# Performance work log

Measured on AMD Instinct MI355X. Metric: run time of the kernel, lower is better.

The kernel has to match this reference:

```python
import jax, jax.numpy as jnp
import numpy as np

D_MODEL = 4096
N_Q_HEAD = 32
N_KV_HEAD = 8
HEAD_DIM = D_MODEL // N_Q_HEAD  # 128
N_REP = N_Q_HEAD // N_KV_HEAD   # 4
B, T = 2, 2048


def _rope_tables(seq_len, head_dim, dtype=jnp.float32):
    # theta_i = 10000^(-2*(i-1)/d) for i=1..d/2  (matches torch.pow(10000, -2*(arange(1,d/2+1)-1)/d))
    i = jnp.arange(head_dim // 2, dtype=dtype)
    theta = jnp.power(10000.0, -2.0 * i / head_dim)
    angles = jnp.outer(jnp.arange(seq_len, dtype=dtype), theta)  # [T, d/2]
    return jnp.cos(angles), jnp.sin(angles)


def _apply_rope(x, cos, sin):
    # x: [B, T, h, HD]; pairs are consecutive elements (view_as_complex semantics)
    B_, T_, h, hd = x.shape
    xp = x.reshape(B_, T_, h, hd // 2, 2)
    xr, xi = xp[..., 0], xp[..., 1]
    c = cos[None, :T_, None, :]
    s = sin[None, :T_, None, :]
    out_r = xr * c - xi * s
    out_i = xr * s + xi * c
    return jnp.stack([out_r, out_i], axis=-1).reshape(B_, T_, h, hd)


def setup_inputs() -> dict:
    key = jax.random.key(0)
    ks = jax.random.split(key, 5)
    scale = 0.02
    x = jax.random.normal(ks[0], (B, T, D_MODEL), dtype=jnp.float32)
    wq = jax.random.normal(ks[1], (D_MODEL, N_Q_HEAD * HEAD_DIM), dtype=jnp.float32) * scale
    wk = jax.random.normal(ks[2], (D_MODEL, N_KV_HEAD * HEAD_DIM), dtype=jnp.float32) * scale
    wv = jax.random.normal(ks[3], (D_MODEL, N_KV_HEAD * HEAD_DIM), dtype=jnp.float32) * scale
    wo = jax.random.normal(ks[4], (N_Q_HEAD * HEAD_DIM, D_MODEL), dtype=jnp.float32) * scale
    # causal mask: 1 where masked (strict upper triangle), per masked_fill(mask==1, -inf)
    attention_mask = jnp.triu(jnp.ones((T, T), dtype=jnp.int32), k=1)
    return {"x": x, "wq": wq, "wk": wk, "wv": wv, "wo": wo, "attention_mask": attention_mask}


def reference(x, wq, wk, wv, wo, attention_mask):
    B_, T_, _ = x.shape
    xq = (x @ wq).reshape(B_, T_, N_Q_HEAD, HEAD_DIM)
    xk = (x @ wk).reshape(B_, T_, N_KV_HEAD, HEAD_DIM)
    xv = (x @ wv).reshape(B_, T_, N_KV_HEAD, HEAD_DIM)

    cos, sin = _rope_tables(T_, HEAD_DIM, x.dtype)
    xq = _apply_rope(xq, cos, sin)
    xk = _apply_rope(xk, cos, sin)

    # GQA: repeat kv heads (training path: no cache)
    xk = jnp.repeat(xk, N_REP, axis=2)  # [B, T, HQ, HD]
    xv = jnp.repeat(xv, N_REP, axis=2)

    q = xq.transpose(0, 2, 1, 3)  # [B, H, T, HD]
    k = xk.transpose(0, 2, 1, 3)
    v = xv.transpose(0, 2, 1, 3)

    scores = jnp.einsum('bhqd,bhkd->bhqk', q, k) / jnp.sqrt(jnp.asarray(HEAD_DIM, x.dtype))
    scores = jnp.where(attention_mask[None, None, :, :] == 1, -jnp.inf, scores)
    probs = jax.nn.softmax(scores, axis=-1)
    out = jnp.einsum('bhqk,bhkd->bhqd', probs, v)
    out = out.transpose(0, 2, 1, 3).reshape(B_, T_, N_Q_HEAD * HEAD_DIM)
    return out @ wo
```

## Files before the change

kernel.cpp:

```cpp
#include <hip/hip_runtime.h>
#include <hip/hip_bf16.h>
#include <math.h>

typedef __hip_bfloat16 bf16;
typedef short bf16x8 __attribute__((ext_vector_type(8)));
typedef float f32x4 __attribute__((ext_vector_type(4)));
typedef unsigned int u32;
typedef unsigned short u16;

#define GLD16(g, l)                                                            \
  __builtin_amdgcn_global_load_lds(                                            \
      (const __attribute__((address_space(1))) void*)(g),                      \
      (__attribute__((address_space(3))) void*)(l), 16, 0, 0)

#define BARRIER() asm volatile("s_barrier" ::: "memory")
#define VMCNT(n) asm volatile("s_waitcnt vmcnt(" #n ")" ::: "memory")

__global__ void convert_f32_bf16(const float* __restrict__ in,
                                 bf16* __restrict__ out) {
  size_t i = ((size_t)blockIdx.x * 256 + threadIdx.x) * 4;
  float4 v = *(const float4*)(in + i);
  out[i + 0] = __float2bfloat16(v.x);
  out[i + 1] = __float2bfloat16(v.y);
  out[i + 2] = __float2bfloat16(v.z);
  out[i + 3] = __float2bfloat16(v.w);
}

__global__ void transpose_f32_bf16(const float* __restrict__ in,
                                   bf16* __restrict__ out, int R, int C) {
  __shared__ bf16 tile[32][33];
  int tx = threadIdx.x & 31, ty = threadIdx.x >> 5;
  int c0 = blockIdx.x * 32, r0 = blockIdx.y * 32;
#pragma unroll
  for (int i = 0; i < 32; i += 8)
    tile[ty + i][tx] = __float2bfloat16(in[(size_t)(r0 + ty + i) * C + c0 + tx]);
  __syncthreads();
#pragma unroll
  for (int i = 0; i < 32; i += 8)
    out[(size_t)(c0 + ty + i) * R + r0 + tx] = tile[tx][ty + i];
}

__global__ void transpose_v(const bf16* __restrict__ V, bf16* __restrict__ VT) {
  __shared__ bf16 tile[32][33];
  int s = blockIdx.z, b = s >> 3, kvh = s & 7;
  int t0 = blockIdx.x * 32, d0 = blockIdx.y * 32;
  int tx = threadIdx.x & 31, ty = threadIdx.x >> 5;
#pragma unroll
  for (int i = 0; i < 32; i += 8)
    tile[ty + i][tx] =
        V[(size_t)(b * 2048 + t0 + ty + i) * 6144 + kvh * 128 + d0 + tx];
  __syncthreads();
#pragma unroll
  for (int i = 0; i < 32; i += 8)
    VT[((size_t)s * 128 + d0 + ty + i) * 2048 + t0 + tx] = tile[tx][ty + i];
}

__global__ void rope_table_k(float* __restrict__ tab) {
  int idx = blockIdx.x * 256 + threadIdx.x;
  int t = idx >> 6, i = idx & 63;
  float theta = powf(10000.0f, -2.0f * (float)i / 128.0f);
  float ang = (float)t * theta;
  tab[idx * 2 + 0] = cosf(ang);
  tab[idx * 2 + 1] = sinf(ang);
}

__global__ void rope_apply(bf16* __restrict__ X, const float* __restrict__ tab,
                           int nheads, int rowstride, float omul) {
  size_t idx = (size_t)blockIdx.x * 256 + threadIdx.x;
  int i = (int)(idx & 63);
  size_t rest = idx >> 6;
  int h = (int)(rest % nheads);
  size_t r = rest / nheads;
  int t = (int)(r & 2047);
  float c = tab[(t * 64 + i) * 2 + 0];
  float s = tab[(t * 64 + i) * 2 + 1];
  bf16* p = X + r * (size_t)rowstride + h * 128 + 2 * i;
  float xr = __bfloat162float(p[0]), xi = __bfloat162float(p[1]);
  p[0] = __float2bfloat16((xr * c - xi * s) * omul);
  p[1] = __float2bfloat16((xr * s + xi * c) * omul);
}

template <typename OutT>
__global__ __launch_bounds__(512, 2) void gemm_bt8(const bf16* __restrict__ A,
                                                   const bf16* __restrict__ BT,
                                                   OutT* __restrict__ C, int M,
                                                   int N, int K) {
  __shared__ bf16 AS[2][2][128 * 64];
  __shared__ bf16 BS[2][2][128 * 64];

  const int tid = threadIdx.x;
  const int lane = tid & 63;
  const int w = tid >> 6, wm = w >> 2, wn = w & 3;
  const int lr = lane & 15, hi = lane >> 4;

  int gx = gridDim.x;
  int nwg = gx * gridDim.y;
  int bid = blockIdx.y * gx + blockIdx.x;
  int swz = (bid & 7) * (nwg >> 3) + (bid >> 3);
  const int m0 = (swz / gx) * 256, n0 = (swz % gx) * 256;

  const int NKT = K >> 6;
  const int NI = K >> 7;
  const int srow = tid >> 3;
  const int scol = ((tid & 7) ^ (srow & 7)) << 3;

  f32x4 acc[8][4];
#pragma unroll
  for (int m = 0; m < 8; ++m)
#pragma unroll
    for (int n = 0; n < 4; ++n)
#pragma unroll
      for (int j = 0; j < 4; ++j) acc[m][n][j] = 0.f;

  auto STAGE_A = [&](int buf, int kt) {
    int kk0 = (kt < NKT) ? kt * 64 : 0;
#pragma unroll
    for (int hs = 0; hs < 4; ++hs) {
      int ha = hs >> 1, sa = hs & 1;
      const bf16* g = A + (size_t)(m0 + ha * 128 + sa * 64 + srow) * K + kk0 + scol;
      GLD16(g, &AS[buf][ha][(sa * 64 + srow) * 64 + (tid & 7) * 8]);
    }
  };
  auto STAGE_B = [&](int buf, int kt, int half) {
    int kk0 = (kt < NKT) ? kt * 64 : 0;
#pragma unroll
    for (int sa = 0; sa < 2; ++sa) {
      const bf16* g =
          BT + (size_t)(n0 + half * 128 + sa * 64 + srow) * K + kk0 + scol;
      GLD16(g, &BS[buf][half][(sa * 64 + srow) * 64 + (tid & 7) * 8]);
    }
  };

  bf16x8 bfr[4][2], af[2][2];
  auto READ_B = [&](int buf) {
#pragma unroll
    for (int n = 0; n < 4; ++n) {
      int row = (wn & 1) * 64 + n * 16 + lr;
#pragma unroll
      for (int kk = 0; kk < 2; ++kk)
        bfr[n][kk] = *(const bf16x8*)(&BS[buf][wn >> 1]
                                         [row * 64 + (((kk * 4 + hi) ^ (row & 7)) << 3)]);
    }
  };
  auto READ_A = [&](int buf, int q) {
#pragma unroll
    for (int mm = 0; mm < 2; ++mm) {
      int row = (q * 2 + mm) * 16 + lr;
#pragma unroll
      for (int kk = 0; kk < 2; ++kk)
        af[mm][kk] = *(const bf16x8*)(&AS[buf][wm]
                                         [row * 64 + (((kk * 4 + hi) ^ (row & 7)) << 3)]);
    }
  };

#define MFMA16(q)                                                              \
  do {                                                                         \
    __builtin_amdgcn_s_setprio(1);                                             \
    _Pragma("unroll") for (int mm = 0; mm < 2; ++mm)                           \
        _Pragma("unroll") for (int n = 0; n < 4; ++n)                          \
        _Pragma("unroll") for (int kk = 0; kk < 2; ++kk)                       \
            acc[(q) * 2 + mm][n] = __builtin_amdgcn_mfma_f32_16x16x32_bf16(    \
                af[mm][kk], bfr[n][kk], acc[(q) * 2 + mm][n], 0, 0, 0);        \
    __builtin_amdgcn_s_setprio(0);                                             \
  } while (0)

  STAGE_A(0, 0);
  STAGE_B(0, 0, 0);
  STAGE_B(0, 0, 1);
  STAGE_B(1, 1, 0);
  STAGE_B(1, 1, 1);
  VMCNT(4);
  BARRIER();

  for (int i = 0; i < NI; ++i) {
    int t = 2 * i;
    READ_B(0); READ_A(0, 0); STAGE_A(1, t + 1);
    BARRIER(); MFMA16(0); BARRIER();
    READ_A(0, 1); STAGE_B(0, t + 2, 0);
    BARRIER(); MFMA16(1); BARRIER();
    READ_A(0, 2); STAGE_B(0, t + 2, 1);
    BARRIER(); MFMA16(2); BARRIER();
    READ_A(0, 3);
    BARRIER(); MFMA16(3); VMCNT(4); BARRIER();
    READ_B(1); READ_A(1, 0); STAGE_A(0, t + 2);
    BARRIER(); MFMA16(0); BARRIER();
    READ_A(1, 1); STAGE_B(1, t + 3, 0);
    BARRIER(); MFMA16(1); BARRIER();
    READ_A(1, 2); STAGE_B(1, t + 3, 1);
    BARRIER(); MFMA16(2); BARRIER();
    READ_A(1, 3);
    BARRIER(); MFMA16(3); VMCNT(4); BARRIER();
  }

  VMCNT(0);
  BARRIER();

#pragma unroll
  for (int m = 0; m < 8; ++m) {
    int row_base = m0 + wm * 128 + m * 16 + hi * 4;
#pragma unroll
    for (int n = 0; n < 4; ++n) {
      int col = n0 + wn * 64 + n * 16 + lr;
#pragma unroll
      for (int j = 0; j < 4; ++j) {
        float v = acc[m][n][j];
        if constexpr (sizeof(OutT) == 2)
          C[(size_t)(row_base + j) * N + col] = (OutT)__float2bfloat16(v);
        else
          C[(size_t)(row_base + j) * N + col] = (OutT)v;
      }
    }
  }
#undef MFMA16
}

static __device__ inline u32 cvtpk_bf16(float a, float b) {
  u32 r;
  asm("v_cvt_pk_bf16_f32 %0, %1, %2" : "=v"(r) : "v"(a), "v"(b));
  return r;
}

__global__ __launch_bounds__(256) void flash_attn2(const bf16* __restrict__ Q,
                                                   const bf16* __restrict__ K,
                                                   const bf16* __restrict__ VT,
                                                   bf16* __restrict__ AO) {
  __shared__ bf16 Kbuf[2][64 * 128];
  __shared__ bf16 Vbuf[2][128 * 64];

  int bid = blockIdx.x;
  int lid = (bid & 7) * 128 + (bid >> 3);
  int qt = 15 - (lid & 15);
  int hq = (lid >> 4) & 3;
  int kvh = (lid >> 6) & 7;
  int b = lid >> 9;
  int h = kvh * 4 + hq;

  const int tid = threadIdx.x;
  const int lane = tid & 63, w = tid >> 6;
  const int lr = lane & 15, hi = lane >> 4;
  const int ko = hi * 8;
  const int qrow0 = qt * 128 + w * 32;
  const int nt = 2 * qt + 2;

  const bf16* Kg0 = K + (size_t)b * 2048 * 6144 + kvh * 128;
  const bf16* Vg0 = VT + (size_t)(b * 8 + kvh) * 128 * 2048;

  bf16x8 qf[2][4];
#pragma unroll
  for (int mi = 0; mi < 2; ++mi) {
    const bf16* qb = Q + (size_t)(b * 2048 + qrow0 + mi * 16 + lr) * 6144 + h * 128;
#pragma unroll
    for (int kk = 0; kk < 4; ++kk) qf[mi][kk] = *(const bf16x8*)(qb + kk * 32 + ko);
  }

  f32x4 O[2][8];
  float m_[2], l_[2];
#pragma unroll
  for (int mi = 0; mi < 2; ++mi) {
    m_[mi] = -1e30f;
    l_[mi] = 0.f;
#pragma unroll
    for (int dd = 0; dd < 8; ++dd)
#pragma unroll
      for (int j = 0; j < 4; ++j) O[mi][dd][j] = 0.f;
  }

  auto STAGE = [&](int buf, int kv0) {
    bf16* Ks = &Kbuf[buf][0];
    bf16* Vs = &Vbuf[buf][0];
    const bf16* Kg = Kg0 + (size_t)kv0 * 6144;
    const bf16* Vg = Vg0 + kv0;
#pragma unroll
    for (int it = 0; it < 4; ++it) {
      int s = it * 256 + tid;
      int row = s >> 4, c = s & 15;
      GLD16(Kg + (size_t)row * 6144 + ((c ^ (row & 7)) << 3), Ks + s * 8);
    }
#pragma unroll
    for (int it = 0; it < 4; ++it) {
      int s = it * 256 + tid;
      int row = s >> 3, c = s & 7;
      GLD16(Vg + (size_t)row * 2048 + ((c ^ (row & 7)) << 3), Vs + s * 8);
    }
  };

  STAGE(0, 0);
  __syncthreads();

  for (int t = 0; t < nt; ++t) {
    int kv0 = t * 64;
    if (t + 1 < nt) STAGE((t + 1) & 1, kv0 + 64);

    if (kv0 <= qrow0 + 31) {
      const bf16* Ks = &Kbuf[t & 1][0];
      const bf16* Vs = &Vbuf[t & 1][0];

      f32x4 Sx[2][4];
#pragma unroll
      for (int mi = 0; mi < 2; ++mi)
#pragma unroll
        for (int cb = 0; cb < 4; ++cb)
#pragma unroll
          for (int j = 0; j < 4; ++j) Sx[mi][cb][j] = 0.f;

      __builtin_amdgcn_s_setprio(1);
#pragma unroll
      for (int cb = 0; cb < 4; ++cb) {
        bf16x8 kf[4];
#pragma unroll
        for (int kk = 0; kk < 4; ++kk)
          kf[kk] = *(const bf16x8*)(Ks + (cb * 16 + lr) * 128 +
                                    (((kk * 4 + hi) ^ (lr & 7)) << 3));
#pragma unroll
        for (int mi = 0; mi < 2; ++mi)
#pragma unroll
          for (int kk = 0; kk < 4; ++kk)
            Sx[mi][cb] = __builtin_amdgcn_mfma_f32_16x16x32_bf16(
                kf[kk], qf[mi][kk], Sx[mi][cb], 0, 0, 0);
      }
      __builtin_amdgcn_s_setprio(0);

      bool domask = (kv0 + 63 > qrow0);
      u32 pau[2][2][4];
#pragma unroll
      for (int mi = 0; mi < 2; ++mi) {
        int q = qrow0 + mi * 16 + lr;
        if (domask) {
#pragma unroll
          for (int cb = 0; cb < 4; ++cb)
#pragma unroll
            for (int j = 0; j < 4; ++j)
              if (kv0 + cb * 16 + hi * 4 + j > q) Sx[mi][cb][j] = -1e30f;
        }
        float pm = -1e30f;
#pragma unroll
        for (int cb = 0; cb < 4; ++cb)
#pragma unroll
          for (int j = 0; j < 4; ++j) pm = fmaxf(pm, Sx[mi][cb][j]);
        pm = fmaxf(pm, __shfl_xor(pm, 16));
        pm = fmaxf(pm, __shfl_xor(pm, 32));

        if (!__all(pm - m_[mi] <= 11.5416f)) {
          float nm = fmaxf(m_[mi], pm);
          float rs = exp2f(m_[mi] - nm);
          m_[mi] = nm;
          l_[mi] *= rs;
#pragma unroll
          for (int dd = 0; dd < 8; ++dd)
#pragma unroll
            for (int j = 0; j < 4; ++j) O[mi][dd][j] *= rs;
        }
        float mcur = m_[mi];
        float ps = 0.f;
#pragma unroll
        for (int cb = 0; cb < 4; ++cb)
#pragma unroll
          for (int j = 0; j < 4; ++j) {
            float p = exp2f(Sx[mi][cb][j] - mcur);
            Sx[mi][cb][j] = p;
            ps += p;
          }
        ps += __shfl_xor(ps, 16);
        ps += __shfl_xor(ps, 32);
        l_[mi] += ps;

        u32 vp[8];
#pragma unroll
        for (int cb = 0; cb < 4; ++cb)
#pragma unroll
          for (int jp = 0; jp < 2; ++jp)
            vp[cb * 2 + jp] = cvtpk_bf16(Sx[mi][cb][2 * jp], Sx[mi][cb][2 * jp + 1]);

#pragma unroll
        for (int kk2 = 0; kk2 < 2; ++kk2)
#pragma unroll
          for (int e = 0; e < 4; ++e) {
            int src = lr + ((hi & 1) << 5) + ((e >> 1) << 4);
            u32 va = (u32)__shfl((int)vp[4 * kk2 + (e & 1)], src);
            u32 vb = (u32)__shfl((int)vp[4 * kk2 + 2 + (e & 1)], src);
            pau[mi][kk2][e] = (hi & 2) ? vb : va;
          }
      }

      __builtin_amdgcn_s_setprio(1);
#pragma unroll
      for (int dd = 0; dd < 8; ++dd) {
        bf16x8 vf[2];
#pragma unroll
        for (int kk2 = 0; kk2 < 2; ++kk2)
          vf[kk2] = *(const bf16x8*)(Vs + (dd * 16 + lr) * 64 +
                                     (((kk2 * 4 + hi) ^ (lr & 7)) << 3));
#pragma unroll
        for (int mi = 0; mi < 2; ++mi)
#pragma unroll
          for (int kk2 = 0; kk2 < 2; ++kk2) {
            union { u32 u[4]; bf16x8 h; } cv;
#pragma unroll
            for (int e = 0; e < 4; ++e) cv.u[e] = pau[mi][kk2][e];
            O[mi][dd] = __builtin_amdgcn_mfma_f32_16x16x32_bf16(
                vf[kk2], cv.h, O[mi][dd], 0, 0, 0);
          }
      }
      __builtin_amdgcn_s_setprio(0);
    }
    __syncthreads();
  }

#pragma unroll
  for (int mi = 0; mi < 2; ++mi) {
    float inv = 1.0f / l_[mi];
    bf16* outp = AO + (size_t)(b * 2048 + qrow0 + mi * 16 + lr) * 4096 + h * 128;
#pragma unroll
    for (int dd = 0; dd < 8; ++dd) {
      union { u16 s[4]; unsigned long long v; } pk;
#pragma unroll
      for (int j = 0; j < 4; ++j)
        pk.s[j] = __bfloat16_as_ushort(__float2bfloat16(O[mi][dd][j] * inv));
      *(unsigned long long*)(outp + dd * 16 + hi * 4) = pk.v;
    }
  }
}

extern "C" void kernel_launch(void* const* d_in, const int* in_sizes, int n_in,
                              void* d_out, int out_size, void* d_ws,
                              size_t ws_size, hipStream_t stream) {
  const float* x = (const float*)d_in[0];
  const float* wq = (const float*)d_in[1];
  const float* wk = (const float*)d_in[2];
  const float* wv = (const float*)d_in[3];
  const float* wo = (const float*)d_in[4];

  char* ws = (char*)d_ws;
  bf16* xb    = (bf16*)(ws + 0);
  bf16* WqkvT = (bf16*)(ws + 33554432);
  bf16* WoT   = (bf16*)(ws + 83886080);
  bf16* QKV   = (bf16*)(ws + 117440512);
  bf16* VTb   = (bf16*)(ws + 167772160);
  float* tab  = (float*)(ws + 176160768);
  bf16* AOb   = xb;

  const float LOG2E = 1.4426950408889634f;
  const float ISQ = 0.08838834764831845f;

  convert_f32_bf16<<<16384, 256, 0, stream>>>(x, xb);
  transpose_f32_bf16<<<dim3(128, 128), 256, 0, stream>>>(wq, WqkvT, 4096, 4096);
  transpose_f32_bf16<<<dim3(32, 128), 256, 0, stream>>>(
      wk, WqkvT + (size_t)4096 * 4096, 4096, 1024);
  transpose_f32_bf16<<<dim3(32, 128), 256, 0, stream>>>(
      wv, WqkvT + (size_t)5120 * 4096, 4096, 1024);
  transpose_f32_bf16<<<dim3(128, 128), 256, 0, stream>>>(wo, WoT, 4096, 4096);
  rope_table_k<<<512, 256, 0, stream>>>(tab);

  gemm_bt8<bf16><<<dim3(24, 16), 512, 0, stream>>>(xb, WqkvT, QKV, 4096, 6144,
                                                   4096);

  rope_apply<<<32768, 256, 0, stream>>>(QKV, tab, 32, 6144, LOG2E * ISQ);
  rope_apply<<<8192, 256, 0, stream>>>(QKV + 4096, tab, 8, 6144, 1.0f);

  transpose_v<<<dim3(64, 4, 16), 256, 0, stream>>>(QKV + 5120, VTb);

  flash_attn2<<<1024, 256, 0, stream>>>(QKV, QKV + 4096, VTb, AOb);

  gemm_bt8<float><<<dim3(16, 16), 512, 0, stream>>>(AOb, WoT, (float*)d_out,
                                                    4096, 4096, 4096);
}
```

Measured before the change: 667.1 us.

## Rewrite flash attention with 32x32x16 MFMA, 256-row query tiles and 512 threads

Replaces the 16x16x32 MFMA attention kernel with one built on 32x32x16 MFMA. Each wave now owns 32 query rows as a single tile, and a block of 8 waves covers 256 query rows with 512 threads, launched as 512 blocks instead of 1024. The aim is to load each staged K/V tile once for twice as many queries and to cut cross-lane shuffles and per-row softmax bookkeeping. In exchange the grid has half as many blocks, causal load balance is coarser, and per-thread register pressure rises.

```diff
diff --git a/kernel.cpp b/kernel.cpp
--- a/kernel.cpp
+++ b/kernel.cpp
@@ -5,6 +5,7 @@
 typedef __hip_bfloat16 bf16;
 typedef short bf16x8 __attribute__((ext_vector_type(8)));
 typedef float f32x4 __attribute__((ext_vector_type(4)));
+typedef float f32x16 __attribute__((ext_vector_type(16)));
 typedef unsigned int u32;
 typedef unsigned short u16;
 
@@ -220,7 +221,7 @@
   return r;
 }
 
-__global__ __launch_bounds__(256) void flash_attn2(const bf16* __restrict__ Q,
+__global__ __launch_bounds__(512) void flash_attn3(const bf16* __restrict__ Q,
                                                    const bf16* __restrict__ K,
                                                    const bf16* __restrict__ VT,
                                                    bf16* __restrict__ AO) {
@@ -228,42 +229,36 @@
   __shared__ bf16 Vbuf[2][128 * 64];
 
   int bid = blockIdx.x;
-  int lid = (bid & 7) * 128 + (bid >> 3);
-  int qt = 15 - (lid & 15);
-  int hq = (lid >> 4) & 3;
-  int kvh = (lid >> 6) & 7;
-  int b = lid >> 9;
+  int b = bid >> 8;
+  int i = (bid >> 3) & 31;
+  int kvh = bid & 7;
+  int hq = i >> 3;
+  int qt = 7 - (i & 7);
   int h = kvh * 4 + hq;
 
   const int tid = threadIdx.x;
   const int lane = tid & 63, w = tid >> 6;
-  const int lr = lane & 15, hi = lane >> 4;
-  const int ko = hi * 8;
-  const int qrow0 = qt * 128 + w * 32;
-  const int nt = 2 * qt + 2;
+  const int ql = lane & 31, hi = lane >> 5;
+  const int qrow0 = qt * 256 + w * 32;
+  const int nt = 4 * qt + 4;
 
   const bf16* Kg0 = K + (size_t)b * 2048 * 6144 + kvh * 128;
   const bf16* Vg0 = VT + (size_t)(b * 8 + kvh) * 128 * 2048;
 
-  bf16x8 qf[2][4];
-#pragma unroll
-  for (int mi = 0; mi < 2; ++mi) {
-    const bf16* qb = Q + (size_t)(b * 2048 + qrow0 + mi * 16 + lr) * 6144 + h * 128;
-#pragma unroll
-    for (int kk = 0; kk < 4; ++kk) qf[mi][kk] = *(const bf16x8*)(qb + kk * 32 + ko);
+  bf16x8 qf[8];
+  {
+    const bf16* qb =
+        Q + (size_t)(b * 2048 + qrow0 + ql) * 6144 + h * 128 + hi * 8;
+#pragma unroll
+    for (int dc = 0; dc < 8; ++dc) qf[dc] = *(const bf16x8*)(qb + dc * 16);
   }
 
-  f32x4 O[2][8];
-  float m_[2], l_[2];
-#pragma unroll
-  for (int mi = 0; mi < 2; ++mi) {
-    m_[mi] = -1e30f;
-    l_[mi] = 0.f;
-#pragma unroll
-    for (int dd = 0; dd < 8; ++dd)
-#pragma unroll
-      for (int j = 0; j < 4; ++j) O[mi][dd][j] = 0.f;
-  }
+  f32x16 O[4];
+#pragma unroll
+  for (int d4 = 0; d4 < 4; ++d4)
+#pragma unroll
+    for (int e = 0; e < 16; ++e) O[d4][e] = 0.f;
+  float m_ = -1e30f, l_ = 0.f;
 
   auto STAGE = [&](int buf, int kv0) {
     bf16* Ks = &Kbuf[buf][0];
@@ -271,14 +266,14 @@
     const bf16* Kg = Kg0 + (size_t)kv0 * 6144;
     const bf16* Vg = Vg0 + kv0;
 #pragma unroll
-    for (int it = 0; it < 4; ++it) {
-      int s = it * 256 + tid;
+    for (int it = 0; it < 2; ++it) {
+      int s = it * 512 + tid;
       int row = s >> 4, c = s & 15;
       GLD16(Kg + (size_t)row * 6144 + ((c ^ (row & 7)) << 3), Ks + s * 8);
     }
 #pragma unroll
-    for (int it = 0; it < 4; ++it) {
-      int s = it * 256 + tid;
+    for (int it = 0; it < 2; ++it) {
+      int s = it * 512 + tid;
       int row = s >> 3, c = s & 7;
       GLD16(Vg + (size_t)row * 2048 + ((c ^ (row & 7)) << 3), Vs + s * 8);
     }
@@ -295,130 +290,115 @@
       const bf16* Ks = &Kbuf[t & 1][0];
       const bf16* Vs = &Vbuf[t & 1][0];
 
-      f32x4 Sx[2][4];
-#pragma unroll
-      for (int mi = 0; mi < 2; ++mi)
-#pragma unroll
-        for (int cb = 0; cb < 4; ++cb)
-#pragma unroll
-          for (int j = 0; j < 4; ++j) Sx[mi][cb][j] = 0.f;
+      f32x16 Sx[2];
+#pragma unroll
+      for (int cb = 0; cb < 2; ++cb)
+#pragma unroll
+        for (int e = 0; e < 16; ++e) Sx[cb][e] = 0.f;
 
       __builtin_amdgcn_s_setprio(1);
 #pragma unroll
-      for (int cb = 0; cb < 4; ++cb) {
-        bf16x8 kf[4];
-#pragma unroll
-        for (int kk = 0; kk < 4; ++kk)
-          kf[kk] = *(const bf16x8*)(Ks + (cb * 16 + lr) * 128 +
-                                    (((kk * 4 + hi) ^ (lr & 7)) << 3));
-#pragma unroll
-        for (int mi = 0; mi < 2; ++mi)
-#pragma unroll
-          for (int kk = 0; kk < 4; ++kk)
-            Sx[mi][cb] = __builtin_amdgcn_mfma_f32_16x16x32_bf16(
-                kf[kk], qf[mi][kk], Sx[mi][cb], 0, 0, 0);
+      for (int cb = 0; cb < 2; ++cb) {
+        int krow = cb * 32 + ql;
+#pragma unroll
+        for (int dc = 0; dc < 8; ++dc) {
+          bf16x8 kf = *(const bf16x8*)(Ks + krow * 128 +
+                                       (((dc * 2 + hi) ^ (ql & 7)) << 3));
+          Sx[cb] = __builtin_amdgcn_mfma_f32_32x32x16_bf16(kf, qf[dc], Sx[cb],
+                                                           0, 0, 0);
+        }
       }
       __builtin_amdgcn_s_setprio(0);
 
+      int q = qrow0 + ql;
       bool domask = (kv0 + 63 > qrow0);
-      u32 pau[2][2][4];
-#pragma unroll
-      for (int mi = 0; mi < 2; ++mi) {
-        int q = qrow0 + mi * 16 + lr;
-        if (domask) {
-#pragma unroll
-          for (int cb = 0; cb < 4; ++cb)
-#pragma unroll
-            for (int j = 0; j < 4; ++j)
-              if (kv0 + cb * 16 + hi * 4 + j > q) Sx[mi][cb][j] = -1e30f;
+      if (domask) {
+#pragma unroll
+        for (int cb = 0; cb < 2; ++cb)
+#pragma unroll
+          for (int r = 0; r < 16; ++r) {
+            int kv = kv0 + cb * 32 + (r & 3) + 8 * (r >> 2) + 4 * hi;
+            if (kv > q) Sx[cb][r] = -1e30f;
+          }
+      }
+      float pm = -1e30f;
+#pragma unroll
+      for (int cb = 0; cb < 2; ++cb)
+#pragma unroll
+        for (int r = 0; r < 16; ++r) pm = fmaxf(pm, Sx[cb][r]);
+      pm = fmaxf(pm, __shfl_xor(pm, 32));
+
+      if (!__all(pm - m_ <= 11.5416f)) {
+        float nm = fmaxf(m_, pm);
+        float rs = exp2f(m_ - nm);
+        m_ = nm;
+        l_ *= rs;
+#pragma unroll
+        for (int d4 = 0; d4 < 4; ++d4)
+#pragma unroll
+          for (int e = 0; e < 16; ++e) O[d4][e] *= rs;
+      }
+      float ps = 0.f;
+#pragma unroll
+      for (int cb = 0; cb < 2; ++cb)
+#pragma unroll
+        for (int r = 0; r < 16; ++r) {
+          float p = exp2f(Sx[cb][r] - m_);
+          Sx[cb][r] = p;
+          ps += p;
         }
-        float pm = -1e30f;
-#pragma unroll
-        for (int cb = 0; cb < 4; ++cb)
-#pragma unroll
-          for (int j = 0; j < 4; ++j) pm = fmaxf(pm, Sx[mi][cb][j]);
-        pm = fmaxf(pm, __shfl_xor(pm, 16));
-        pm = fmaxf(pm, __shfl_xor(pm, 32));
-
-        if (!__all(pm - m_[mi] <= 11.5416f)) {
-          float nm = fmaxf(m_[mi], pm);
-          float rs = exp2f(m_[mi] - nm);
-          m_[mi] = nm;
-          l_[mi] *= rs;
-#pragma unroll
-          for (int dd = 0; dd < 8; ++dd)
-#pragma unroll
-            for (int j = 0; j < 4; ++j) O[mi][dd][j] *= rs;
+      ps += __shfl_xor(ps, 32);
+      l_ += ps;
+
+      bf16x8 pb[4];
+#pragma unroll
+      for (int kb = 0; kb < 4; ++kb) {
+        int cb = kb >> 1, r0 = 8 * (kb & 1);
+        u32 Av = cvtpk_bf16(Sx[cb][r0 + 0], Sx[cb][r0 + 1]);
+        u32 Bv = cvtpk_bf16(Sx[cb][r0 + 2], Sx[cb][r0 + 3]);
+        u32 Cv = cvtpk_bf16(Sx[cb][r0 + 4], Sx[cb][r0 + 5]);
+        u32 Dv = cvtpk_bf16(Sx[cb][r0 + 6], Sx[cb][r0 + 7]);
+        u32 sA = (u32)__shfl_xor((int)Av, 32);
+        u32 sB = (u32)__shfl_xor((int)Bv, 32);
+        u32 sC = (u32)__shfl_xor((int)Cv, 32);
+        u32 sD = (u32)__shfl_xor((int)Dv, 32);
+        union { u32 u[4]; bf16x8 v; } pk;
+        pk.u[0] = hi ? sC : Av;
+        pk.u[1] = hi ? sD : Bv;
+        pk.u[2] = hi ? Cv : sA;
+        pk.u[3] = hi ? Dv : sB;
+        pb[kb] = pk.v;
+      }
+
+      __builtin_amdgcn_s_setprio(1);
+#pragma unroll
+      for (int d4 = 0; d4 < 4; ++d4) {
+        int vrow = d4 * 32 + ql;
+#pragma unroll
+        for (int kb = 0; kb < 4; ++kb) {
+          bf16x8 vf = *(const bf16x8*)(Vs + vrow * 64 +
+                                       (((kb * 2 + hi) ^ (ql & 7)) << 3));
+          O[d4] = __builtin_amdgcn_mfma_f32_32x32x16_bf16(vf, pb[kb], O[d4], 0,
+                                                          0, 0);
         }
-        float mcur = m_[mi];
-        float ps = 0.f;
-#pragma unroll
-        for (int cb = 0; cb < 4; ++cb)
-#pragma unroll
-          for (int j = 0; j < 4; ++j) {
-            float p = exp2f(Sx[mi][cb][j] - mcur);
-            Sx[mi][cb][j] = p;
-            ps += p;
-          }
-        ps += __shfl_xor(ps, 16);
-        ps += __shfl_xor(ps, 32);
-        l_[mi] += ps;
-
-        u32 vp[8];
-#pragma unroll
-        for (int cb = 0; cb < 4; ++cb)
-#pragma unroll
-          for (int jp = 0; jp < 2; ++jp)
-            vp[cb * 2 + jp] = cvtpk_bf16(Sx[mi][cb][2 * jp], Sx[mi][cb][2 * jp + 1]);
-
-#pragma unroll
-        for (int kk2 = 0; kk2 < 2; ++kk2)
-#pragma unroll
-          for (int e = 0; e < 4; ++e) {
-            int src = lr + ((hi & 1) << 5) + ((e >> 1) << 4);
-            u32 va = (u32)__shfl((int)vp[4 * kk2 + (e & 1)], src);
-            u32 vb = (u32)__shfl((int)vp[4 * kk2 + 2 + (e & 1)], src);
-            pau[mi][kk2][e] = (hi & 2) ? vb : va;
-          }
-      }
-
-      __builtin_amdgcn_s_setprio(1);
-#pragma unroll
-      for (int dd = 0; dd < 8; ++dd) {
-        bf16x8 vf[2];
-#pragma unroll
-        for (int kk2 = 0; kk2 < 2; ++kk2)
-          vf[kk2] = *(const bf16x8*)(Vs + (dd * 16 + lr) * 64 +
-                                     (((kk2 * 4 + hi) ^ (lr & 7)) << 3));
-#pragma unroll
-        for (int mi = 0; mi < 2; ++mi)
-#pragma unroll
-          for (int kk2 = 0; kk2 < 2; ++kk2) {
-            union { u32 u[4]; bf16x8 h; } cv;
-#pragma unroll
-            for (int e = 0; e < 4; ++e) cv.u[e] = pau[mi][kk2][e];
-            O[mi][dd] = __builtin_amdgcn_mfma_f32_16x16x32_bf16(
-                vf[kk2], cv.h, O[mi][dd], 0, 0, 0);
-          }
       }
       __builtin_amdgcn_s_setprio(0);
     }
     __syncthreads();
   }
 
-#pragma unroll
-  for (int mi = 0; mi < 2; ++mi) {
-    float inv = 1.0f / l_[mi];
-    bf16* outp = AO + (size_t)(b * 2048 + qrow0 + mi * 16 + lr) * 4096 + h * 128;
-#pragma unroll
-    for (int dd = 0; dd < 8; ++dd) {
+  float inv = 1.0f / l_;
+  bf16* outp = AO + (size_t)(b * 2048 + qrow0 + ql) * 4096 + h * 128;
+#pragma unroll
+  for (int d4 = 0; d4 < 4; ++d4)
+#pragma unroll
+    for (int rg = 0; rg < 4; ++rg) {
       union { u16 s[4]; unsigned long long v; } pk;
 #pragma unroll
       for (int j = 0; j < 4; ++j)
-        pk.s[j] = __bfloat16_as_ushort(__float2bfloat16(O[mi][dd][j] * inv));
-      *(unsigned long long*)(outp + dd * 16 + hi * 4) = pk.v;
-    }
-  }
+        pk.s[j] = __bfloat16_as_ushort(__float2bfloat16(O[d4][rg * 4 + j] * inv));
+      *(unsigned long long*)(outp + d4 * 32 + rg * 8 + hi * 4) = pk.v;
+    }
 }
 
 extern "C" void kernel_launch(void* const* d_in, const int* in_sizes, int n_in,
@@ -459,7 +439,7 @@
 
   transpose_v<<<dim3(64, 4, 16), 256, 0, stream>>>(QKV + 5120, VTb);
 
-  flash_attn2<<<1024, 256, 0, stream>>>(QKV, QKV + 4096, VTb, AOb);
+  flash_attn3<<<512, 512, 0, stream>>>(QKV, QKV + 4096, VTb, AOb);
 
   gemm_bt8<float><<<dim3(16, 16), 512, 0, stream>>>(AOb, WoT, (float*)d_out,
                                                     4096, 4096, 4096);
```

Result: faster. 619.0 us (-7.2%).
